# Kernel tuning notes

Measured on AMD Instinct MI355X. Metric: run time of the kernel, lower is better.

The kernel has to match this reference:

```python
import jax, jax.numpy as jnp
import numpy as np

BN_EPS = 1e-5
GRID_W = 17  # conv output width hardcoded via lat_idx*17+lon_idx

def _conv(x, w, b, stride):
    y = jax.lax.conv_general_dilated(x, w, (stride, stride), [(1, 1), (1, 1)],
                                     dimension_numbers=("NCHW", "OIHW", "NCHW"))
    return y + b[None, :, None, None]

def _bn_eval(x, g, b):
    # running_mean=0, running_var=1 (fresh BatchNorm in eval mode)
    inv = jnp.float32(1.0 / np.sqrt(1.0 + BN_EPS))
    return x * (g[None, :, None, None] * inv) + b[None, :, None, None]

def setup_inputs() -> dict:
    key = jax.random.key(0)
    ks = iter(jax.random.split(key, 64))
    def rn(shape, s=0.05):
        return jax.random.normal(next(ks), shape, jnp.float32) * s
    B, S, K = 512, 128, 64
    NR = 100000
    inp = {}
    inp["roads"] = jax.random.randint(next(ks), (B, S), 0, NR)
    inp["ratios"] = jax.random.uniform(next(ks), (B, S), jnp.float32) * 0.9 + 0.1
    inp["T"] = jax.random.normal(next(ks), (1, 1, 138, 138), jnp.float32)
    inp["lon_idx"] = jax.random.randint(next(ks), (B, K), 0, 17)
    inp["lat_idx"] = jax.random.randint(next(ks), (B, K), 0, 17)
    inp["lengths"] = jax.random.uniform(next(ks), (NR,), jnp.float32) * 100.0 + 1.0
    inp["map_u"] = jnp.arange(NR, dtype=jnp.int32)
    inp["map_s1"] = jax.random.randint(next(ks), (NR,), 0, 14)
    inp["map_s2"] = jax.random.randint(next(ks), (NR,), 0, 7)
    inp["map_s3"] = jax.random.randint(next(ks), (NR,), 0, 2)
    inp["emb_u"] = rn((NR, 128))
    inp["emb_s1"] = rn((14, 16)); inp["emb_s2"] = rn((7, 8)); inp["emb_s3"] = rn((2, 4))
    inp["rho_w1"] = rn((156, 512)); inp["rho_b1"] = jnp.zeros((512,), jnp.float32)
    inp["rho_w21"] = rn((512, 128)); inp["rho_b21"] = jnp.zeros((128,), jnp.float32)
    inp["conv1_w"] = rn((32, 1, 5, 5)); inp["conv1_b"] = jnp.zeros((32,), jnp.float32)
    inp["bn1_g"] = jnp.ones((32,), jnp.float32); inp["bn1_b"] = jnp.zeros((32,), jnp.float32)
    inp["conv2_w"] = rn((64, 32, 4, 4)); inp["conv2_b"] = jnp.zeros((64,), jnp.float32)
    inp["bn2_g"] = jnp.ones((64,), jnp.float32); inp["bn2_b"] = jnp.zeros((64,), jnp.float32)
    inp["conv3_w"] = rn((128, 64, 4, 4)); inp["conv3_b"] = jnp.zeros((128,), jnp.float32)
    inp["bn3_g"] = jnp.ones((128,), jnp.float32); inp["bn3_b"] = jnp.zeros((128,), jnp.float32)
    inp["f2_w1"] = rn((128, 256)); inp["f2_b1"] = jnp.zeros((256,), jnp.float32)
    inp["f2_w2"] = rn((256, 128)); inp["f2_b2"] = jnp.zeros((128,), jnp.float32)
    inp["f_w1"] = rn((256, 512)); inp["f_b1"] = jnp.zeros((512,), jnp.float32)
    inp["f_w21"] = rn((512, 1)); inp["f_b21"] = jnp.zeros((1,), jnp.float32)
    inp["f_w22"] = rn((512, 1)); inp["f_b22"] = jnp.zeros((1,), jnp.float32)
    return inp

def reference(roads, ratios, T, lon_idx, lat_idx, lengths, map_u, map_s1, map_s2, map_s3,
              emb_u, emb_s1, emb_s2, emb_s3, rho_w1, rho_b1, rho_w21, rho_b21,
              conv1_w, conv1_b, bn1_g, bn1_b, conv2_w, conv2_b, bn2_g, bn2_b,
              conv3_w, conv3_b, bn3_g, bn3_b, f2_w1, f2_b1, f2_w2, f2_b2,
              f_w1, f_b1, f_w21, f_b21, f_w22, f_b22):
    # road lengths / weights
    road_lens = lengths[roads] * ratios               # (B,S)
    l = road_lens.sum(axis=1)                         # (B,)
    w = road_lens / l[:, None]                        # (B,S)
    # ProbRho (eval: dropout=id, reparameterize -> mu)
    u = emb_u[map_u[roads]]                           # (B,S,128)
    s1 = emb_s1[map_s1[roads]]; s2 = emb_s2[map_s2[roads]]; s3 = emb_s3[map_s3[roads]]
    x = jnp.concatenate([u, s1, s2, s3], axis=2)      # (B,S,156)
    h = jax.nn.relu(x @ rho_w1 + rho_b1)
    rho = h @ rho_w21 + rho_b21                       # (B,S,128)
    # ProbTraffic_spatial conv stack
    t = jax.nn.leaky_relu(_bn_eval(_conv(T, conv1_w, conv1_b, 2), bn1_g, bn1_b), 0.1)
    t = jax.nn.leaky_relu(_bn_eval(_conv(t, conv2_w, conv2_b, 2), bn2_g, bn2_b), 0.1)
    t = jax.nn.leaky_relu(_bn_eval(_conv(t, conv3_w, conv3_b, 2), bn3_g, bn3_b), 0.1)  # (1,128,17,17)
    c_flat = jnp.transpose(t[0], (1, 2, 0)).reshape(-1, t.shape[1])  # (289,128)
    # fused segment gather + mean over each trajectory's grid cells
    idx = lat_idx * GRID_W + lon_idx                  # (B,K)
    c_mean = c_flat[idx].mean(axis=1)                 # (B,128)
    h2 = jax.nn.selu(c_mean @ f2_w1 + f2_b1)
    c2 = h2 @ f2_w2 + f2_b2                           # (B,128)
    # ProbTravelTime
    xcat = jnp.concatenate([rho, jnp.broadcast_to(c2[:, None, :], rho.shape)], axis=2)  # (B,S,256)
    h3 = jax.nn.relu(xcat @ f_w1 + f_b1)              # (B,S,512)
    logm = (h3 @ f_w21 + f_b21)[..., 0]               # (B,S)
    logv = (h3 @ f_w22 + f_b22)[..., 0]
    logw = jnp.log(w)
    logm_agg = jax.nn.logsumexp(logm + logw, axis=1)
    logv_agg = jax.nn.logsumexp(logv + 2.0 * logw, axis=1)
    logl = jnp.log(l)
    logmu = logl - logm_agg
    loglam = logl - 3.0 * logm_agg - logv_agg
    return (logmu, loglam)
```

## Files before the change

kernel.cpp:

```cpp
#include <hip/hip_runtime.h>
#include <hip/hip_bf16.h>
#include <math.h>

#define BB 512
#define SS 128
#define NROWS (BB*SS)
#define TMG 128
#define NBLKG (NROWS/TMG)

__device__ __forceinline__ float leaky01(float x){ return x >= 0.f ? x : 0.1f*x; }

#define BN_INV 0.9999950000374997f
#define SELU_A 1.6732632423543772f
#define SELU_S 1.0507009873554805f

typedef __attribute__((ext_vector_type(8))) short short8;
typedef __attribute__((ext_vector_type(4))) float f32x4;

__device__ __forceinline__ unsigned short f2bf(float f) {
    unsigned int u = __float_as_uint(f);
    u += 0x7fff + ((u >> 16) & 1);
    return (unsigned short)(u >> 16);
}
__device__ __forceinline__ unsigned int pk2(float a, float b) {
    __hip_bfloat162 h = __float22bfloat162_rn(make_float2(a, b));
    unsigned int u;
    __builtin_memcpy(&u, &h, 4);
    return u;
}
__device__ __forceinline__ uint2 pack4bf(float a, float b, float c, float d) {
    uint2 r; r.x = pk2(a, b); r.y = pk2(c, d); return r;
}

__device__ __forceinline__ unsigned short* xsp(unsigned short* base, int row, int col) {
    unsigned off = (unsigned)(row*384 + col*2);
    off ^= (unsigned)((row & 7) << 4);
    return (unsigned short*)((char*)base + off);
}
__device__ __forceinline__ unsigned short* h1p(unsigned short* base, int row, int col) {
    unsigned off = (unsigned)(row*1024 + col*2);
    off ^= (unsigned)((row & 7) << 4);
    return (unsigned short*)((char*)base + off);
}
__device__ __forceinline__ unsigned short* xcp(unsigned short* base, int row, int col) {
    unsigned off = (unsigned)(row*256 + col*2);
    off ^= (unsigned)((row & 7) << 4);
    return (unsigned short*)((char*)base + off);
}

#define PREP_N (278528 + 32768 + 131072)
#define PREP_BLOCKS (PREP_N/256)
#define CONV1_BLOCKS 578

__global__ __launch_bounds__(256) void combo1_kernel(
    const float* __restrict__ w1, const float* __restrict__ w21, const float* __restrict__ fw1,
    unsigned short* __restrict__ sw1, unsigned short* __restrict__ sw21, unsigned short* __restrict__ sw3,
    const float* __restrict__ c2w_in, const float* __restrict__ c3w_in,
    float* __restrict__ w2t, float* __restrict__ w3t,
    const float* __restrict__ T, const float* __restrict__ cw,
    const float* __restrict__ cbias, const float* __restrict__ g,
    const float* __restrict__ bb, float* __restrict__ out)
{
    if (blockIdx.x < PREP_BLOCKS) {
        int t = blockIdx.x*256 + threadIdx.x;
        if (t < 81920) {
            int j = t & 7; int r = t >> 3; int lane = r & 63; r >>= 6;
            int ks = r % 5; int nt = r / 5;
            int n = nt*16 + (lane & 15);
            int k = ks*32 + (lane >> 4)*8 + j;
            float v = (k < 156) ? w1[k*512 + n] : 0.f;
            sw1[t] = f2bf(v);
        } else if (t < 147456) {
            int u = t - 81920;
            int j = u & 7; int r = u >> 3; int lane = r & 63; r >>= 6;
            int ks = r & 15; int nt = r >> 4;
            int d = nt*16 + (lane & 15);
            int k = ks*32 + (lane >> 4)*8 + j;
            sw21[u] = f2bf(w21[k*128 + d]);
        } else if (t < 278528) {
            int u = t - 147456;
            int j = u & 7; int r = u >> 3; int lane = r & 63; r >>= 6;
            int ks = r & 7; int nt = r >> 3;
            int n = nt*16 + (lane & 15);
            int k = ks*32 + (lane >> 4)*8 + j;
            sw3[u] = f2bf(fw1[k*512 + n]);
        } else if (t < 278528 + 32768) {
            int u = t - 278528;
            int oc = u >> 9; int r = u & 511;
            int kk = r >> 5; int ic = r & 31;
            w2t[u] = c2w_in[oc*512 + ic*16 + kk];
        } else {
            int u = t - (278528 + 32768);
            int oc = u >> 10; int r = u & 1023;
            int kk = r >> 6; int ic = r & 63;
            w3t[u] = c3w_in[oc*1024 + ic*16 + kk];
        }
    } else {
        int t = (blockIdx.x - PREP_BLOCKS)*256 + threadIdx.x;
        if (t >= 32*68*68) return;
        int oc  = t & 31;
        int pos = t >> 5;
        int oy = pos / 68, ox = pos % 68;
        float acc = cbias[oc];
        #pragma unroll
        for (int ky=0; ky<5; ++ky) {
            int iy = oy*2 - 1 + ky;
            if (iy < 0 || iy >= 138) continue;
            #pragma unroll
            for (int kx=0; kx<5; ++kx) {
                int ix = ox*2 - 1 + kx;
                if (ix < 0 || ix >= 138) continue;
                acc += cw[oc*25 + ky*5 + kx] * T[iy*138 + ix];
            }
        }
        acc = acc * (g[oc]*BN_INV) + bb[oc];
        out[pos*32 + oc] = leaky01(acc);
    }
}

__global__ __launch_bounds__(256) void conv2_kernel(
    const float* __restrict__ in,
    const float* __restrict__ w2t,
    const float* __restrict__ bias, const float* __restrict__ g,
    const float* __restrict__ bb, float* __restrict__ out)
{
    int gid = blockIdx.x*256 + threadIdx.x;
    if (gid >= 64*34*34*4) return;
    int icg = gid & 3;
    int o   = gid >> 2;
    int oc  = o & 63;
    int pos = o >> 6;
    int oy = pos / 34, ox = pos % 34;
    float acc = 0.f;
    #pragma unroll
    for (int ky=0; ky<4; ++ky) {
        int iy = oy*2 - 1 + ky;
        if (iy < 0 || iy >= 68) continue;
        #pragma unroll
        for (int kx=0; kx<4; ++kx) {
            int ix = ox*2 - 1 + kx;
            if (ix < 0 || ix >= 68) continue;
            const float* ip = &in[(iy*68+ix)*32 + icg*8];
            const float* wp = &w2t[oc*512 + (ky*4+kx)*32 + icg*8];
            float4 i0 = *(const float4*)ip, i1 = *(const float4*)(ip+4);
            float4 w0 = *(const float4*)wp, w1v = *(const float4*)(wp+4);
            acc += i0.x*w0.x + i0.y*w0.y + i0.z*w0.z + i0.w*w0.w
                 + i1.x*w1v.x + i1.y*w1v.y + i1.z*w1v.z + i1.w*w1v.w;
        }
    }
    acc += __shfl_xor(acc, 1, 64);
    acc += __shfl_xor(acc, 2, 64);
    if (icg == 0) {
        acc = (acc + bias[oc]) * (g[oc]*BN_INV) + bb[oc];
        out[pos*64 + oc] = leaky01(acc);
    }
}

__global__ __launch_bounds__(256) void conv3_kernel(
    const float* __restrict__ in,
    const float* __restrict__ w3t,
    const float* __restrict__ bias, const float* __restrict__ g,
    const float* __restrict__ bb, float* __restrict__ outT)
{
    int gid = blockIdx.x*256 + threadIdx.x;
    if (gid >= 128*289*8) return;
    int icg = gid & 7;
    int o   = gid >> 3;
    int oc  = o & 127;
    int pos = o >> 7;
    int oy = pos / 17, ox = pos % 17;
    float acc = 0.f;
    #pragma unroll
    for (int ky=0; ky<4; ++ky) {
        int iy = oy*2 - 1 + ky;
        if (iy < 0 || iy >= 34) continue;
        #pragma unroll
        for (int kx=0; kx<4; ++kx) {
            int ix = ox*2 - 1 + kx;
            if (ix < 0 || ix >= 34) continue;
            const float* ip = &in[(iy*34+ix)*64 + icg*8];
            const float* wp = &w3t[oc*1024 + (ky*4+kx)*64 + icg*8];
            float4 i0 = *(const float4*)ip, i1 = *(const float4*)(ip+4);
            float4 w0 = *(const float4*)wp, w1v = *(const float4*)(wp+4);
            acc += i0.x*w0.x + i0.y*w0.y + i0.z*w0.z + i0.w*w0.w
                 + i1.x*w1v.x + i1.y*w1v.y + i1.z*w1v.z + i1.w*w1v.w;
        }
    }
    acc += __shfl_xor(acc, 1, 64);
    acc += __shfl_xor(acc, 2, 64);
    acc += __shfl_xor(acc, 4, 64);
    if (icg == 0) {
        acc = (acc + bias[oc]) * (g[oc]*BN_INV) + bb[oc];
        outT[pos*128 + oc] = leaky01(acc);
    }
}

__global__ __launch_bounds__(256) void cmh2c2_kernel(
    const float* __restrict__ t3T, const int* __restrict__ lat, const int* __restrict__ lon,
    const float* __restrict__ w1, const float* __restrict__ b1,
    const float* __restrict__ w2, const float* __restrict__ b2,
    const float* __restrict__ fw1, const float* __restrict__ fb1,
    float* __restrict__ cvb)
{
    __shared__ int   ps[64];
    __shared__ float part[256];
    __shared__ float cms[128];
    __shared__ float h2s[256];
    __shared__ float c2s[128];
    const int b = blockIdx.x;
    const int tid = threadIdx.x;
    if (tid < 64) ps[tid] = lat[b*64+tid]*17 + lon[b*64+tid];
    __syncthreads();
    {
        int d = tid & 127, half = tid >> 7;
        float s = 0.f;
        #pragma unroll 8
        for (int k=0; k<32; ++k) s += t3T[ps[half*32+k]*128 + d];
        part[tid] = s;
    }
    __syncthreads();
    if (tid < 128) cms[tid] = (part[tid] + part[tid+128]) * (1.f/64.f);
    __syncthreads();
    {
        float acc = b1[tid];
        #pragma unroll 8
        for (int k=0; k<128; ++k) acc += cms[k] * w1[k*256 + tid];
        h2s[tid] = acc > 0.f ? SELU_S*acc : SELU_S*SELU_A*(expf(acc)-1.f);
    }
    __syncthreads();
    {
        int d = tid & 127, half = tid >> 7;
        float acc = 0.f;
        #pragma unroll 8
        for (int k=0; k<128; ++k) acc += h2s[half*128 + k] * w2[(half*128+k)*128 + d];
        part[tid] = acc;
    }
    __syncthreads();
    if (tid < 128) c2s[tid] = part[tid] + part[tid+128] + b2[tid];
    __syncthreads();
    {
        float a0 = fb1[tid], a1 = fb1[tid + 256];
        #pragma unroll 8
        for (int k=0; k<128; ++k) {
            float c = c2s[k];
            a0 += c * fw1[(128+k)*512 + tid];
            a1 += c * fw1[(128+k)*512 + 256 + tid];
        }
        cvb[b*512 + tid]       = a0;
        cvb[b*512 + 256 + tid] = a1;
    }
}

__global__ __launch_bounds__(1024, 4) void mega_kernel(
    const int* __restrict__ roads, const float* __restrict__ ratios,
    const float* __restrict__ lengths,
    const int* __restrict__ map_u, const int* __restrict__ map_s1,
    const int* __restrict__ map_s2, const int* __restrict__ map_s3,
    const float* __restrict__ emb_u, const float* __restrict__ emb_s1,
    const float* __restrict__ emb_s2, const float* __restrict__ emb_s3,
    const unsigned short* __restrict__ sw1, const float* __restrict__ b1,
    const unsigned short* __restrict__ sw21, const float* __restrict__ b21,
    const unsigned short* __restrict__ sw3, const float* __restrict__ cvb,
    const float* __restrict__ fw21, const float* __restrict__ fb21,
    const float* __restrict__ fw22, const float* __restrict__ fb22,
    float* __restrict__ out)
{
    __shared__ unsigned short buf[65536];
    float* pmv = (float*)buf;
    float* fin = (float*)buf + 4096;

    const int tid  = threadIdx.x;
    const int wid  = tid >> 6;
    const int lane = tid & 63;
    const int lo   = lane & 15;
    const int hi   = lane >> 4;
    const int b    = blockIdx.x;
    const int r0   = b * TMG;
    const int nt2  = wid >> 1;
    const int rh   = wid & 1;

    short8 afp00 = *(const short8*)&sw1[((wid*2+0)*5 + 0)*512 + lane*8];
    short8 afp10 = *(const short8*)&sw1[((wid*2+1)*5 + 0)*512 + lane*8];
    short8 afp01 = *(const short8*)&sw1[((wid*2+0)*5 + 1)*512 + lane*8];
    short8 afp11 = *(const short8*)&sw1[((wid*2+1)*5 + 1)*512 + lane*8];

    {
        int row = tid >> 3, seg = tid & 7;
        int road = roads[r0 + row];
        const float* src = emb_u + (long)map_u[road]*128 + seg*16;
        #pragma unroll
        for (int i=0;i<4;++i) {
            float4 v = *(const float4*)&src[i*4];
            *(uint2*)xsp(buf, row, seg*16 + i*4) = pack4bf(v.x, v.y, v.z, v.w);
        }
    }
    for (int idx = tid; idx < 128*32; idx += 1024) {
        int row = idx >> 5, k2 = idx & 31;
        int road = roads[r0 + row];
        float v;
        if      (k2 < 16) v = emb_s1[map_s1[road]*16 + k2];
        else if (k2 < 24) v = emb_s2[map_s2[road]*8  + (k2-16)];
        else if (k2 < 28) v = emb_s3[map_s3[road]*4  + (k2-24)];
        else              v = 0.f;
        *xsp(buf, row, 128 + k2) = f2bf(v);
    }
    __syncthreads();

    f32x4 acc1[2][8];
    {
        #pragma unroll
        for (int mt=0;mt<2;++mt)
            #pragma unroll
            for (int rg=0;rg<8;++rg) acc1[mt][rg]=(f32x4)(0.f);
        short8 a0c = afp00, a1c = afp10, a0n = afp01, a1n = afp11;
        #pragma unroll
        for (int ks=0; ks<5; ++ks) {
            short8 a0f = a0c, a1f = a1c;
            if (ks < 3) {
                a0f = *(const short8*)&sw1[((wid*2+0)*5 + ks+2)*512 + lane*8];
                a1f = *(const short8*)&sw1[((wid*2+1)*5 + ks+2)*512 + lane*8];
            }
            const int kb = ks*32 + hi*8;
            short8 bf[4];
            #pragma unroll
            for (int rg=0;rg<4;++rg) bf[rg] = *(const short8*)xsp(buf, rg*16+lo, kb);
            #pragma unroll
            for (int rg=0;rg<4;++rg) {
                acc1[0][rg] = __builtin_amdgcn_mfma_f32_16x16x32_bf16(a0c, bf[rg], acc1[0][rg], 0,0,0);
                acc1[1][rg] = __builtin_amdgcn_mfma_f32_16x16x32_bf16(a1c, bf[rg], acc1[1][rg], 0,0,0);
            }
            #pragma unroll
            for (int rg=0;rg<4;++rg) bf[rg] = *(const short8*)xsp(buf, (4+rg)*16+lo, kb);
            #pragma unroll
            for (int rg=0;rg<4;++rg) {
                acc1[0][4+rg] = __builtin_amdgcn_mfma_f32_16x16x32_bf16(a0c, bf[rg], acc1[0][4+rg], 0,0,0);
                acc1[1][4+rg] = __builtin_amdgcn_mfma_f32_16x16x32_bf16(a1c, bf[rg], acc1[1][4+rg], 0,0,0);
            }
            a0c = a0n; a1c = a1n; a0n = a0f; a1n = a1f;
        }
    }
    __syncthreads();

    short8 a2q0, a2q1, a2q2, a2q3;
    {
        a2q0 = *(const short8*)&sw21[(nt2*16 + 0)*512 + lane*8];
        a2q1 = *(const short8*)&sw21[(nt2*16 + 1)*512 + lane*8];
        a2q2 = *(const short8*)&sw21[(nt2*16 + 2)*512 + lane*8];
        a2q3 = *(const short8*)&sw21[(nt2*16 + 3)*512 + lane*8];
        const int n0 = wid * 32;
        #pragma unroll
        for (int mt=0;mt<2;++mt) {
            const int nb = n0 + mt*16 + hi*4;
            float4 bias = *(const float4*)&b1[nb];
            const float* bp = (const float*)&bias;
            #pragma unroll
            for (int rg=0;rg<8;++rg) {
                const float* a = (const float*)&acc1[mt][rg];
                float y0 = fmaxf(a[0]+bp[0], 0.f), y1 = fmaxf(a[1]+bp[1], 0.f);
                float y2 = fmaxf(a[2]+bp[2], 0.f), y3 = fmaxf(a[3]+bp[3], 0.f);
                *(uint2*)h1p(buf, rg*16+lo, nb) = pack4bf(y0,y1,y2,y3);
            }
        }
    }
    __syncthreads();

    f32x4 acc2[4];
    {
        #pragma unroll
        for (int i=0;i<4;++i) acc2[i]=(f32x4)(0.f);
        #pragma unroll
        for (int ks=0; ks<16; ++ks) {
            short8 a_use = a2q0;
            a2q0 = a2q1; a2q1 = a2q2; a2q2 = a2q3;
            if (ks < 12)
                a2q3 = *(const short8*)&sw21[(nt2*16 + ks+4)*512 + lane*8];
            const int kb = ks*32 + hi*8;
            short8 bf[4];
            #pragma unroll
            for (int i=0;i<4;++i) bf[i] = *(const short8*)h1p(buf, (rh*4+i)*16+lo, kb);
            #pragma unroll
            for (int i=0;i<4;++i)
                acc2[i] = __builtin_amdgcn_mfma_f32_16x16x32_bf16(a_use, bf[i], acc2[i], 0,0,0);
        }
    }
    __syncthreads();

    short8 a3c0, a3c1, a3n0, a3n1;
    {
        a3c0 = *(const short8*)&sw3[((wid*2+0)*8 + 0)*512 + lane*8];
        a3c1 = *(const short8*)&sw3[((wid*2+1)*8 + 0)*512 + lane*8];
        a3n0 = *(const short8*)&sw3[((wid*2+0)*8 + 1)*512 + lane*8];
        a3n1 = *(const short8*)&sw3[((wid*2+1)*8 + 1)*512 + lane*8];
        const int nb = nt2*16 + hi*4;
        float4 bias = *(const float4*)&b21[nb];
        const float* bp = (const float*)&bias;
        #pragma unroll
        for (int i=0;i<4;++i) {
            const float* a = (const float*)&acc2[i];
            *(uint2*)xcp(buf, (rh*4+i)*16+lo, nb) =
                pack4bf(a[0]+bp[0], a[1]+bp[1], a[2]+bp[2], a[3]+bp[3]);
        }
    }
    __syncthreads();

    float sm[8], sv[8];
    {
        const int n0 = wid * 32;
        f32x4 acc[2][8];
        #pragma unroll
        for (int mt=0;mt<2;++mt)
            #pragma unroll
            for (int rg=0;rg<8;++rg) acc[mt][rg]=(f32x4)(0.f);
        #pragma unroll
        for (int ks=0; ks<4; ++ks) {
            short8 c0f = a3c0, c1f = a3c1;
            if (ks < 2) {
                c0f = *(const short8*)&sw3[((wid*2+0)*8 + ks+2)*512 + lane*8];
                c1f = *(const short8*)&sw3[((wid*2+1)*8 + ks+2)*512 + lane*8];
            }
            const int kb = ks*32 + hi*8;
            short8 bf[4];
            #pragma unroll
            for (int rg=0;rg<4;++rg) bf[rg] = *(const short8*)xcp(buf, rg*16+lo, kb);
            #pragma unroll
            for (int rg=0;rg<4;++rg) {
                acc[0][rg] = __builtin_amdgcn_mfma_f32_16x16x32_bf16(a3c0, bf[rg], acc[0][rg], 0,0,0);
                acc[1][rg] = __builtin_amdgcn_mfma_f32_16x16x32_bf16(a3c1, bf[rg], acc[1][rg], 0,0,0);
            }
            #pragma unroll
            for (int rg=0;rg<4;++rg) bf[rg] = *(const short8*)xcp(buf, (4+rg)*16+lo, kb);
            #pragma unroll
            for (int rg=0;rg<4;++rg) {
                acc[0][4+rg] = __builtin_amdgcn_mfma_f32_16x16x32_bf16(a3c0, bf[rg], acc[0][4+rg], 0,0,0);
                acc[1][4+rg] = __builtin_amdgcn_mfma_f32_16x16x32_bf16(a3c1, bf[rg], acc[1][4+rg], 0,0,0);
            }
            a3c0 = a3n0; a3c1 = a3n1; a3n0 = c0f; a3n1 = c1f;
        }
        #pragma unroll
        for (int rg=0;rg<8;++rg){ sm[rg]=0.f; sv[rg]=0.f; }
        #pragma unroll
        for (int mt=0;mt<2;++mt) {
            const int nb = n0 + mt*16 + hi*4;
            float4 bias = *(const float4*)&cvb[b*512 + nb];
            float4 wm   = *(const float4*)&fw21[nb];
            float4 wv   = *(const float4*)&fw22[nb];
            const float *bp=(const float*)&bias, *wmp=(const float*)&wm, *wvp=(const float*)&wv;
            #pragma unroll
            for (int rg=0;rg<8;++rg) {
                const float* a = (const float*)&acc[mt][rg];
                #pragma unroll
                for (int j=0;j<4;++j) {
                    float y = fmaxf(a[j]+bp[j], 0.f);
                    sm[rg] += y*wmp[j];
                    sv[rg] += y*wvp[j];
                }
            }
        }
        #pragma unroll
        for (int rg=0;rg<8;++rg) {
            sm[rg] += __shfl_xor(sm[rg], 16, 64); sm[rg] += __shfl_xor(sm[rg], 32, 64);
            sv[rg] += __shfl_xor(sv[rg], 16, 64); sv[rg] += __shfl_xor(sv[rg], 32, 64);
        }
    }
    __syncthreads();
    if (hi == 0) {
        #pragma unroll
        for (int rg=0;rg<8;++rg) {
            pmv[wid*128 + rg*16 + lo]        = sm[rg];
            pmv[2048 + wid*128 + rg*16 + lo] = sv[rg];
        }
    }
    __syncthreads();

    float rl = 0.f, am = 0.f, av = 0.f;
    if (tid < 128) {
        float s_m = 0.f, s_v = 0.f;
        #pragma unroll
        for (int w=0; w<16; ++w) {
            s_m += pmv[w*128 + tid];
            s_v += pmv[2048 + w*128 + tid];
        }
        s_m += fb21[0]; s_v += fb22[0];
        int gi = r0 + tid;
        rl = lengths[roads[gi]] * ratios[gi];
        float ws = rl;
        #pragma unroll
        for (int off=32; off; off>>=1) ws += __shfl_xor(ws, off, 64);
        if (lane == 0) fin[wid] = ws;
        am = s_m; av = s_v;
    }
    __syncthreads();
    if (tid < 128) {
        float l = fin[0] + fin[1];
        float logl = logf(l);
        float lw = logf(rl) - logl;
        am += lw; av += 2.f*lw;
        float mm = am, mv = av;
        #pragma unroll
        for (int off=32; off; off>>=1) { mm = fmaxf(mm, __shfl_xor(mm, off, 64)); mv = fmaxf(mv, __shfl_xor(mv, off, 64)); }
        if (lane == 0) { fin[2+wid] = mm; fin[4+wid] = mv; fin[8+wid] = logl; }
    }
    __syncthreads();
    if (tid < 128) {
        float mm = fmaxf(fin[2], fin[3]);
        float mv = fmaxf(fin[4], fin[5]);
        float se = expf(am - mm), sev = expf(av - mv);
        #pragma unroll
        for (int off=32; off; off>>=1) { se += __shfl_xor(se, off, 64); sev += __shfl_xor(sev, off, 64); }
        if (lane == 0) { fin[10+wid] = se; fin[12+wid] = sev; }
    }
    __syncthreads();
    if (tid == 0) {
        float mm = fmaxf(fin[2], fin[3]);
        float mv = fmaxf(fin[4], fin[5]);
        float lsem = logf(fin[10] + fin[11]) + mm;
        float lsev = logf(fin[12] + fin[13]) + mv;
        float logl = fin[8];
        out[b]       = logl - lsem;
        out[512 + b] = logl - 3.f*lsem - lsev;
    }
}

extern "C" void kernel_launch(void* const* d_in, const int* in_sizes, int n_in,
                              void* d_out, int out_size, void* d_ws, size_t ws_size,
                              hipStream_t stream) {
    const int*   roads   = (const int*)  d_in[0];
    const float* ratios  = (const float*)d_in[1];
    const float* T       = (const float*)d_in[2];
    const int*   lon_idx = (const int*)  d_in[3];
    const int*   lat_idx = (const int*)  d_in[4];
    const float* lengths = (const float*)d_in[5];
    const int*   map_u   = (const int*)  d_in[6];
    const int*   map_s1  = (const int*)  d_in[7];
    const int*   map_s2  = (const int*)  d_in[8];
    const int*   map_s3  = (const int*)  d_in[9];
    const float* emb_u   = (const float*)d_in[10];
    const float* emb_s1  = (const float*)d_in[11];
    const float* emb_s2  = (const float*)d_in[12];
    const float* emb_s3  = (const float*)d_in[13];
    const float* rho_w1  = (const float*)d_in[14];
    const float* rho_b1  = (const float*)d_in[15];
    const float* rho_w21 = (const float*)d_in[16];
    const float* rho_b21 = (const float*)d_in[17];
    const float* conv1_w = (const float*)d_in[18];
    const float* conv1_b = (const float*)d_in[19];
    const float* bn1_g   = (const float*)d_in[20];
    const float* bn1_b   = (const float*)d_in[21];
    const float* conv2_w = (const float*)d_in[22];
    const float* conv2_b = (const float*)d_in[23];
    const float* bn2_g   = (const float*)d_in[24];
    const float* bn2_b   = (const float*)d_in[25];
    const float* conv3_w = (const float*)d_in[26];
    const float* conv3_b = (const float*)d_in[27];
    const float* bn3_g   = (const float*)d_in[28];
    const float* bn3_b   = (const float*)d_in[29];
    const float* f2_w1   = (const float*)d_in[30];
    const float* f2_b1   = (const float*)d_in[31];
    const float* f2_w2   = (const float*)d_in[32];
    const float* f2_b2   = (const float*)d_in[33];
    const float* f_w1    = (const float*)d_in[34];
    const float* f_b1    = (const float*)d_in[35];
    const float* f_w21   = (const float*)d_in[36];
    const float* f_b21   = (const float*)d_in[37];
    const float* f_w22   = (const float*)d_in[38];
    const float* f_b22   = (const float*)d_in[39];

    float* ws    = (float*)d_ws;
    float* t1    = ws;
    float* t2    = t1 + 147968;
    float* t3T   = t2 + 73984;
    float* cvb   = t3T + 36992;
    float* w2t   = cvb + 262144;
    float* w3t   = w2t + 32768;
    unsigned short* sw1  = (unsigned short*)(w3t + 131072);
    unsigned short* sw21 = sw1 + 81920;
    unsigned short* sw3  = sw21 + 65536;

    combo1_kernel<<<PREP_BLOCKS + CONV1_BLOCKS, 256, 0, stream>>>(
        rho_w1, rho_w21, f_w1, sw1, sw21, sw3,
        conv2_w, conv3_w, w2t, w3t,
        T, conv1_w, conv1_b, bn1_g, bn1_b, t1);
    conv2_kernel<<<(64*34*34*4 + 255)/256, 256, 0, stream>>>(t1, w2t, conv2_b, bn2_g, bn2_b, t2);
    conv3_kernel<<<(128*289*8 + 255)/256, 256, 0, stream>>>(t2, w3t, conv3_b, bn3_g, bn3_b, t3T);
    cmh2c2_kernel<<<512, 256, 0, stream>>>(t3T, lat_idx, lon_idx, f2_w1, f2_b1, f2_w2, f2_b2,
                                           f_w1, f_b1, cvb);
    mega_kernel<<<NBLKG, 1024, 0, stream>>>(roads, ratios, lengths,
                                            map_u, map_s1, map_s2, map_s3,
                                            emb_u, emb_s1, emb_s2, emb_s3,
                                            sw1, rho_b1, sw21, rho_b21,
                                            sw3, cvb, f_w21, f_b21, f_w22, f_b22,
                                            (float*)d_out);
}
```

Measured before the change: 117.1 us.

## Retile per-wave MFMA work into square 64x64 output tiles across GEMMs

Each wave now computes a 4x4 tile of 16x16 outputs (four weight fragments by four row groups, covering half the 128 rows) instead of 2 weight fragments across all 8 row groups. GEMM2 switches to a 2x2 tile per wave. This cuts LDS B-fragment reads per MFMA, since each loaded fragment is reused by four weight fragments. The cross-wave partial reduction and scratch layout are reindexed to match. The trade-off is more weight-fragment registers in flight and a reworked prefetch schedule.

```diff
diff --git a/kernel.cpp b/kernel.cpp
--- a/kernel.cpp
+++ b/kernel.cpp
@@ -267,7 +267,7 @@
 {
     __shared__ unsigned short buf[65536];
     float* pmv = (float*)buf;
-    float* fin = (float*)buf + 4096;
+    float* fin = (float*)buf + 2048;
 
     const int tid  = threadIdx.x;
     const int wid  = tid >> 6;
@@ -276,13 +276,15 @@
     const int hi   = lane >> 4;
     const int b    = blockIdx.x;
     const int r0   = b * TMG;
-    const int nt2  = wid >> 1;
-    const int rh   = wid & 1;
-
-    short8 afp00 = *(const short8*)&sw1[((wid*2+0)*5 + 0)*512 + lane*8];
-    short8 afp10 = *(const short8*)&sw1[((wid*2+1)*5 + 0)*512 + lane*8];
-    short8 afp01 = *(const short8*)&sw1[((wid*2+0)*5 + 1)*512 + lane*8];
-    short8 afp11 = *(const short8*)&sw1[((wid*2+1)*5 + 1)*512 + lane*8];
+    const int ntg  = wid >> 1;
+    const int rhalf= wid & 1;
+    const int ntg2 = wid & 3;
+    const int rq   = wid >> 2;
+
+    short8 afc[4];
+    #pragma unroll
+    for (int mt=0;mt<4;++mt)
+        afc[mt] = *(const short8*)&sw1[((ntg*4+mt)*5 + 0)*512 + lane*8];
 
     {
         int row = tid >> 3, seg = tid & 7;
@@ -306,179 +308,177 @@
     }
     __syncthreads();
 
-    f32x4 acc1[2][8];
-    {
-        #pragma unroll
-        for (int mt=0;mt<2;++mt)
-            #pragma unroll
-            for (int rg=0;rg<8;++rg) acc1[mt][rg]=(f32x4)(0.f);
-        short8 a0c = afp00, a1c = afp10, a0n = afp01, a1n = afp11;
+    f32x4 acc1[4][4];
+    {
+        #pragma unroll
+        for (int mt=0;mt<4;++mt)
+            #pragma unroll
+            for (int rt=0;rt<4;++rt) acc1[mt][rt]=(f32x4)(0.f);
         #pragma unroll
         for (int ks=0; ks<5; ++ks) {
-            short8 a0f = a0c, a1f = a1c;
-            if (ks < 3) {
-                a0f = *(const short8*)&sw1[((wid*2+0)*5 + ks+2)*512 + lane*8];
-                a1f = *(const short8*)&sw1[((wid*2+1)*5 + ks+2)*512 + lane*8];
+            short8 afn[4];
+            if (ks < 4) {
+                #pragma unroll
+                for (int mt=0;mt<4;++mt)
+                    afn[mt] = *(const short8*)&sw1[((ntg*4+mt)*5 + ks+1)*512 + lane*8];
             }
             const int kb = ks*32 + hi*8;
             short8 bf[4];
             #pragma unroll
-            for (int rg=0;rg<4;++rg) bf[rg] = *(const short8*)xsp(buf, rg*16+lo, kb);
-            #pragma unroll
-            for (int rg=0;rg<4;++rg) {
-                acc1[0][rg] = __builtin_amdgcn_mfma_f32_16x16x32_bf16(a0c, bf[rg], acc1[0][rg], 0,0,0);
-                acc1[1][rg] = __builtin_amdgcn_mfma_f32_16x16x32_bf16(a1c, bf[rg], acc1[1][rg], 0,0,0);
-            }
-            #pragma unroll
-            for (int rg=0;rg<4;++rg) bf[rg] = *(const short8*)xsp(buf, (4+rg)*16+lo, kb);
-            #pragma unroll
-            for (int rg=0;rg<4;++rg) {
-                acc1[0][4+rg] = __builtin_amdgcn_mfma_f32_16x16x32_bf16(a0c, bf[rg], acc1[0][4+rg], 0,0,0);
-                acc1[1][4+rg] = __builtin_amdgcn_mfma_f32_16x16x32_bf16(a1c, bf[rg], acc1[1][4+rg], 0,0,0);
-            }
-            a0c = a0n; a1c = a1n; a0n = a0f; a1n = a1f;
-        }
-    }
-    __syncthreads();
-
-    short8 a2q0, a2q1, a2q2, a2q3;
-    {
-        a2q0 = *(const short8*)&sw21[(nt2*16 + 0)*512 + lane*8];
-        a2q1 = *(const short8*)&sw21[(nt2*16 + 1)*512 + lane*8];
-        a2q2 = *(const short8*)&sw21[(nt2*16 + 2)*512 + lane*8];
-        a2q3 = *(const short8*)&sw21[(nt2*16 + 3)*512 + lane*8];
-        const int n0 = wid * 32;
-        #pragma unroll
-        for (int mt=0;mt<2;++mt) {
-            const int nb = n0 + mt*16 + hi*4;
+            for (int rt=0;rt<4;++rt)
+                bf[rt] = *(const short8*)xsp(buf, (rhalf*4+rt)*16+lo, kb);
+            #pragma unroll
+            for (int mt=0;mt<4;++mt)
+                #pragma unroll
+                for (int rt=0;rt<4;++rt)
+                    acc1[mt][rt] = __builtin_amdgcn_mfma_f32_16x16x32_bf16(afc[mt], bf[rt], acc1[mt][rt], 0,0,0);
+            if (ks < 4) {
+                #pragma unroll
+                for (int mt=0;mt<4;++mt) afc[mt] = afn[mt];
+            }
+        }
+    }
+    __syncthreads();
+
+    short8 a2c0, a2c1, a2n0, a2n1;
+    {
+        a2c0 = *(const short8*)&sw21[((ntg2*2+0)*16 + 0)*512 + lane*8];
+        a2c1 = *(const short8*)&sw21[((ntg2*2+1)*16 + 0)*512 + lane*8];
+        a2n0 = *(const short8*)&sw21[((ntg2*2+0)*16 + 1)*512 + lane*8];
+        a2n1 = *(const short8*)&sw21[((ntg2*2+1)*16 + 1)*512 + lane*8];
+        #pragma unroll
+        for (int mt=0;mt<4;++mt) {
+            const int nb = (ntg*4+mt)*16 + hi*4;
             float4 bias = *(const float4*)&b1[nb];
             const float* bp = (const float*)&bias;
             #pragma unroll
-            for (int rg=0;rg<8;++rg) {
-                const float* a = (const float*)&acc1[mt][rg];
+            for (int rt=0;rt<4;++rt) {
+                const float* a = (const float*)&acc1[mt][rt];
                 float y0 = fmaxf(a[0]+bp[0], 0.f), y1 = fmaxf(a[1]+bp[1], 0.f);
                 float y2 = fmaxf(a[2]+bp[2], 0.f), y3 = fmaxf(a[3]+bp[3], 0.f);
-                *(uint2*)h1p(buf, rg*16+lo, nb) = pack4bf(y0,y1,y2,y3);
-            }
-        }
-    }
-    __syncthreads();
-
-    f32x4 acc2[4];
-    {
-        #pragma unroll
-        for (int i=0;i<4;++i) acc2[i]=(f32x4)(0.f);
-        #pragma unroll
+                *(uint2*)h1p(buf, (rhalf*4+rt)*16+lo, nb) = pack4bf(y0,y1,y2,y3);
+            }
+        }
+    }
+    __syncthreads();
+
+    f32x4 acc2[2][2];
+    {
+        acc2[0][0]=(f32x4)(0.f); acc2[0][1]=(f32x4)(0.f);
+        acc2[1][0]=(f32x4)(0.f); acc2[1][1]=(f32x4)(0.f);
+        #pragma unroll 4
         for (int ks=0; ks<16; ++ks) {
-            short8 a_use = a2q0;
-            a2q0 = a2q1; a2q1 = a2q2; a2q2 = a2q3;
-            if (ks < 12)
-                a2q3 = *(const short8*)&sw21[(nt2*16 + ks+4)*512 + lane*8];
+            short8 u0 = a2c0, u1 = a2c1;
+            a2c0 = a2n0; a2c1 = a2n1;
+            if (ks < 14) {
+                a2n0 = *(const short8*)&sw21[((ntg2*2+0)*16 + ks+2)*512 + lane*8];
+                a2n1 = *(const short8*)&sw21[((ntg2*2+1)*16 + ks+2)*512 + lane*8];
+            }
+            const int kb = ks*32 + hi*8;
+            short8 bf0 = *(const short8*)h1p(buf, (rq*2+0)*16+lo, kb);
+            short8 bf1 = *(const short8*)h1p(buf, (rq*2+1)*16+lo, kb);
+            acc2[0][0] = __builtin_amdgcn_mfma_f32_16x16x32_bf16(u0, bf0, acc2[0][0], 0,0,0);
+            acc2[0][1] = __builtin_amdgcn_mfma_f32_16x16x32_bf16(u0, bf1, acc2[0][1], 0,0,0);
+            acc2[1][0] = __builtin_amdgcn_mfma_f32_16x16x32_bf16(u1, bf0, acc2[1][0], 0,0,0);
+            acc2[1][1] = __builtin_amdgcn_mfma_f32_16x16x32_bf16(u1, bf1, acc2[1][1], 0,0,0);
+        }
+    }
+    __syncthreads();
+
+    short8 a3c[4];
+    {
+        #pragma unroll
+        for (int mt=0;mt<4;++mt)
+            a3c[mt] = *(const short8*)&sw3[((ntg*4+mt)*8 + 0)*512 + lane*8];
+        #pragma unroll
+        for (int mt=0;mt<2;++mt) {
+            const int nb = (ntg2*2+mt)*16 + hi*4;
+            float4 bias = *(const float4*)&b21[nb];
+            const float* bp = (const float*)&bias;
+            #pragma unroll
+            for (int rt=0;rt<2;++rt) {
+                const float* a = (const float*)&acc2[mt][rt];
+                *(uint2*)xcp(buf, (rq*2+rt)*16+lo, nb) =
+                    pack4bf(a[0]+bp[0], a[1]+bp[1], a[2]+bp[2], a[3]+bp[3]);
+            }
+        }
+    }
+    __syncthreads();
+
+    float sm[4], sv[4];
+    {
+        f32x4 acc[4][4];
+        #pragma unroll
+        for (int mt=0;mt<4;++mt)
+            #pragma unroll
+            for (int rt=0;rt<4;++rt) acc[mt][rt]=(f32x4)(0.f);
+        #pragma unroll
+        for (int ks=0; ks<4; ++ks) {
+            short8 a3n[4];
+            if (ks < 3) {
+                #pragma unroll
+                for (int mt=0;mt<4;++mt)
+                    a3n[mt] = *(const short8*)&sw3[((ntg*4+mt)*8 + ks+1)*512 + lane*8];
+            }
             const int kb = ks*32 + hi*8;
             short8 bf[4];
             #pragma unroll
-            for (int i=0;i<4;++i) bf[i] = *(const short8*)h1p(buf, (rh*4+i)*16+lo, kb);
-            #pragma unroll
-            for (int i=0;i<4;++i)
-                acc2[i] = __builtin_amdgcn_mfma_f32_16x16x32_bf16(a_use, bf[i], acc2[i], 0,0,0);
-        }
-    }
-    __syncthreads();
-
-    short8 a3c0, a3c1, a3n0, a3n1;
-    {
-        a3c0 = *(const short8*)&sw3[((wid*2+0)*8 + 0)*512 + lane*8];
-        a3c1 = *(const short8*)&sw3[((wid*2+1)*8 + 0)*512 + lane*8];
-        a3n0 = *(const short8*)&sw3[((wid*2+0)*8 + 1)*512 + lane*8];
-        a3n1 = *(const short8*)&sw3[((wid*2+1)*8 + 1)*512 + lane*8];
-        const int nb = nt2*16 + hi*4;
-        float4 bias = *(const float4*)&b21[nb];
-        const float* bp = (const float*)&bias;
-        #pragma unroll
-        for (int i=0;i<4;++i) {
-            const float* a = (const float*)&acc2[i];
-            *(uint2*)xcp(buf, (rh*4+i)*16+lo, nb) =
-                pack4bf(a[0]+bp[0], a[1]+bp[1], a[2]+bp[2], a[3]+bp[3]);
-        }
-    }
-    __syncthreads();
-
-    float sm[8], sv[8];
-    {
-        const int n0 = wid * 32;
-        f32x4 acc[2][8];
-        #pragma unroll
-        for (int mt=0;mt<2;++mt)
-            #pragma unroll
-            for (int rg=0;rg<8;++rg) acc[mt][rg]=(f32x4)(0.f);
-        #pragma unroll
-        for (int ks=0; ks<4; ++ks) {
-            short8 c0f = a3c0, c1f = a3c1;
-            if (ks < 2) {
-                c0f = *(const short8*)&sw3[((wid*2+0)*8 + ks+2)*512 + lane*8];
-                c1f = *(const short8*)&sw3[((wid*2+1)*8 + ks+2)*512 + lane*8];
-            }
-            const int kb = ks*32 + hi*8;
-            short8 bf[4];
-            #pragma unroll
-            for (int rg=0;rg<4;++rg) bf[rg] = *(const short8*)xcp(buf, rg*16+lo, kb);
-            #pragma unroll
-            for (int rg=0;rg<4;++rg) {
-                acc[0][rg] = __builtin_amdgcn_mfma_f32_16x16x32_bf16(a3c0, bf[rg], acc[0][rg], 0,0,0);
-                acc[1][rg] = __builtin_amdgcn_mfma_f32_16x16x32_bf16(a3c1, bf[rg], acc[1][rg], 0,0,0);
-            }
-            #pragma unroll
-            for (int rg=0;rg<4;++rg) bf[rg] = *(const short8*)xcp(buf, (4+rg)*16+lo, kb);
-            #pragma unroll
-            for (int rg=0;rg<4;++rg) {
-                acc[0][4+rg] = __builtin_amdgcn_mfma_f32_16x16x32_bf16(a3c0, bf[rg], acc[0][4+rg], 0,0,0);
-                acc[1][4+rg] = __builtin_amdgcn_mfma_f32_16x16x32_bf16(a3c1, bf[rg], acc[1][4+rg], 0,0,0);
-            }
-            a3c0 = a3n0; a3c1 = a3n1; a3n0 = c0f; a3n1 = c1f;
-        }
-        #pragma unroll
-        for (int rg=0;rg<8;++rg){ sm[rg]=0.f; sv[rg]=0.f; }
-        #pragma unroll
-        for (int mt=0;mt<2;++mt) {
-            const int nb = n0 + mt*16 + hi*4;
+            for (int rt=0;rt<4;++rt)
+                bf[rt] = *(const short8*)xcp(buf, (rhalf*4+rt)*16+lo, kb);
+            #pragma unroll
+            for (int mt=0;mt<4;++mt)
+                #pragma unroll
+                for (int rt=0;rt<4;++rt)
+                    acc[mt][rt] = __builtin_amdgcn_mfma_f32_16x16x32_bf16(a3c[mt], bf[rt], acc[mt][rt], 0,0,0);
+            if (ks < 3) {
+                #pragma unroll
+                for (int mt=0;mt<4;++mt) a3c[mt] = a3n[mt];
+            }
+        }
+        #pragma unroll
+        for (int rt=0;rt<4;++rt){ sm[rt]=0.f; sv[rt]=0.f; }
+        #pragma unroll
+        for (int mt=0;mt<4;++mt) {
+            const int nb = (ntg*4+mt)*16 + hi*4;
             float4 bias = *(const float4*)&cvb[b*512 + nb];
             float4 wm   = *(const float4*)&fw21[nb];
             float4 wv   = *(const float4*)&fw22[nb];
             const float *bp=(const float*)&bias, *wmp=(const float*)&wm, *wvp=(const float*)&wv;
             #pragma unroll
-            for (int rg=0;rg<8;++rg) {
-                const float* a = (const float*)&acc[mt][rg];
+            for (int rt=0;rt<4;++rt) {
+                const float* a = (const float*)&acc[mt][rt];
                 #pragma unroll
                 for (int j=0;j<4;++j) {
                     float y = fmaxf(a[j]+bp[j], 0.f);
-                    sm[rg] += y*wmp[j];
-                    sv[rg] += y*wvp[j];
+                    sm[rt] += y*wmp[j];
+                    sv[rt] += y*wvp[j];
                 }
             }
         }
         #pragma unroll
-        for (int rg=0;rg<8;++rg) {
-            sm[rg] += __shfl_xor(sm[rg], 16, 64); sm[rg] += __shfl_xor(sm[rg], 32, 64);
-            sv[rg] += __shfl_xor(sv[rg], 16, 64); sv[rg] += __shfl_xor(sv[rg], 32, 64);
+        for (int rt=0;rt<4;++rt) {
+            sm[rt] += __shfl_xor(sm[rt], 16, 64); sm[rt] += __shfl_xor(sm[rt], 32, 64);
+            sv[rt] += __shfl_xor(sv[rt], 16, 64); sv[rt] += __shfl_xor(sv[rt], 32, 64);
         }
     }
     __syncthreads();
     if (hi == 0) {
         #pragma unroll
-        for (int rg=0;rg<8;++rg) {
-            pmv[wid*128 + rg*16 + lo]        = sm[rg];
-            pmv[2048 + wid*128 + rg*16 + lo] = sv[rg];
+        for (int rt=0;rt<4;++rt) {
+            pmv[wid*64 + rt*16 + lo]        = sm[rt];
+            pmv[1024 + wid*64 + rt*16 + lo] = sv[rt];
         }
     }
     __syncthreads();
 
     float rl = 0.f, am = 0.f, av = 0.f;
     if (tid < 128) {
+        const int rhr = tid >> 6, rr = tid & 63;
         float s_m = 0.f, s_v = 0.f;
         #pragma unroll
-        for (int w=0; w<16; ++w) {
-            s_m += pmv[w*128 + tid];
-            s_v += pmv[2048 + w*128 + tid];
+        for (int k=0; k<8; ++k) {
+            s_m += pmv[(k*2+rhr)*64 + rr];
+            s_v += pmv[1024 + (k*2+rhr)*64 + rr];
         }
         s_m += fb21[0]; s_v += fb22[0];
         int gi = r0 + tid;
```

After: 128.8 us. 1.1x slower.

## Batch four trajectories per block in cmh2c2 to reuse weight loads

Applied to the files above, without the earlier changes.

The grid-feature MLP kernel now handles four batch rows per block, so each weight element loaded from global memory is reused across four accumulators instead of being re-read by 512 separate blocks. This cuts weight traffic for the f2_w1, f2_w2 and f_w1 matvecs by about four times, in exchange for fewer blocks (128) and more registers per thread. Separately, mega_kernel's launch bounds minimum-blocks hint is lowered from 4 to 2, which lets the compiler use more registers per thread at the cost of occupancy.

```diff
diff --git a/kernel.cpp b/kernel.cpp
--- a/kernel.cpp
+++ b/kernel.cpp
@@ -195,6 +195,7 @@
     }
 }
 
+#define BPB 4
 __global__ __launch_bounds__(256) void cmh2c2_kernel(
     const float* __restrict__ t3T, const int* __restrict__ lat, const int* __restrict__ lon,
     const float* __restrict__ w1, const float* __restrict__ b1,
@@ -202,56 +203,87 @@
     const float* __restrict__ fw1, const float* __restrict__ fb1,
     float* __restrict__ cvb)
 {
-    __shared__ int   ps[64];
-    __shared__ float part[256];
-    __shared__ float cms[128];
-    __shared__ float h2s[256];
-    __shared__ float c2s[128];
-    const int b = blockIdx.x;
+    __shared__ int   ps[BPB*64];
+    __shared__ float cms[BPB*128];
+    __shared__ float h2s[BPB*256];
+    __shared__ float part[BPB*2*128];
+    __shared__ float c2s[BPB*128];
+    const int b0 = blockIdx.x * BPB;
     const int tid = threadIdx.x;
-    if (tid < 64) ps[tid] = lat[b*64+tid]*17 + lon[b*64+tid];
-    __syncthreads();
-    {
-        int d = tid & 127, half = tid >> 7;
+    if (tid < BPB*64) {
+        int bl = tid >> 6, k = tid & 63;
+        ps[tid] = lat[(b0+bl)*64+k]*17 + lon[(b0+bl)*64+k];
+    }
+    __syncthreads();
+    #pragma unroll
+    for (int it=0; it<BPB/2; ++it) {
+        int idx = tid + it*256;
+        int bl = idx >> 7, d = idx & 127;
         float s = 0.f;
         #pragma unroll 8
-        for (int k=0; k<32; ++k) s += t3T[ps[half*32+k]*128 + d];
-        part[tid] = s;
-    }
-    __syncthreads();
-    if (tid < 128) cms[tid] = (part[tid] + part[tid+128]) * (1.f/64.f);
-    __syncthreads();
-    {
-        float acc = b1[tid];
-        #pragma unroll 8
-        for (int k=0; k<128; ++k) acc += cms[k] * w1[k*256 + tid];
-        h2s[tid] = acc > 0.f ? SELU_S*acc : SELU_S*SELU_A*(expf(acc)-1.f);
+        for (int k=0; k<64; ++k) s += t3T[ps[bl*64+k]*128 + d];
+        cms[bl*128 + d] = s * (1.f/64.f);
+    }
+    __syncthreads();
+    {
+        int n = tid;
+        float acc[BPB];
+        float bb0 = b1[n];
+        #pragma unroll
+        for (int bl=0;bl<BPB;++bl) acc[bl] = bb0;
+        for (int k=0; k<128; ++k) {
+            float w = w1[k*256 + n];
+            #pragma unroll
+            for (int bl=0;bl<BPB;++bl) acc[bl] += cms[bl*128+k] * w;
+        }
+        #pragma unroll
+        for (int bl=0;bl<BPB;++bl)
+            h2s[bl*256 + n] = acc[bl] > 0.f ? SELU_S*acc[bl] : SELU_S*SELU_A*(expf(acc[bl])-1.f);
     }
     __syncthreads();
     {
         int d = tid & 127, half = tid >> 7;
-        float acc = 0.f;
-        #pragma unroll 8
-        for (int k=0; k<128; ++k) acc += h2s[half*128 + k] * w2[(half*128+k)*128 + d];
-        part[tid] = acc;
-    }
-    __syncthreads();
-    if (tid < 128) c2s[tid] = part[tid] + part[tid+128] + b2[tid];
-    __syncthreads();
-    {
-        float a0 = fb1[tid], a1 = fb1[tid + 256];
-        #pragma unroll 8
+        float acc[BPB];
+        #pragma unroll
+        for (int bl=0;bl<BPB;++bl) acc[bl] = 0.f;
         for (int k=0; k<128; ++k) {
-            float c = c2s[k];
-            a0 += c * fw1[(128+k)*512 + tid];
-            a1 += c * fw1[(128+k)*512 + 256 + tid];
-        }
-        cvb[b*512 + tid]       = a0;
-        cvb[b*512 + 256 + tid] = a1;
-    }
-}
-
-__global__ __launch_bounds__(1024, 4) void mega_kernel(
+            float w = w2[(half*128+k)*128 + d];
+            #pragma unroll
+            for (int bl=0;bl<BPB;++bl) acc[bl] += h2s[bl*256 + half*128 + k] * w;
+        }
+        #pragma unroll
+        for (int bl=0;bl<BPB;++bl) part[(bl*2+half)*128 + d] = acc[bl];
+    }
+    __syncthreads();
+    for (int idx = tid; idx < BPB*128; idx += 256) {
+        int bl = idx >> 7, d = idx & 127;
+        c2s[idx] = part[(bl*2+0)*128 + d] + part[(bl*2+1)*128 + d] + b2[d];
+    }
+    __syncthreads();
+    {
+        float a0[BPB], a1[BPB];
+        float f0 = fb1[tid], f1 = fb1[tid + 256];
+        #pragma unroll
+        for (int bl=0;bl<BPB;++bl){ a0[bl]=f0; a1[bl]=f1; }
+        for (int k=0; k<128; ++k) {
+            float w0 = fw1[(128+k)*512 + tid];
+            float w1v= fw1[(128+k)*512 + 256 + tid];
+            #pragma unroll
+            for (int bl=0;bl<BPB;++bl) {
+                float c = c2s[bl*128+k];
+                a0[bl] += c * w0;
+                a1[bl] += c * w1v;
+            }
+        }
+        #pragma unroll
+        for (int bl=0;bl<BPB;++bl) {
+            cvb[(b0+bl)*512 + tid]       = a0[bl];
+            cvb[(b0+bl)*512 + 256 + tid] = a1[bl];
+        }
+    }
+}
+
+__global__ __launch_bounds__(1024, 2) void mega_kernel(
     const int* __restrict__ roads, const float* __restrict__ ratios,
     const float* __restrict__ lengths,
     const int* __restrict__ map_u, const int* __restrict__ map_s1,
@@ -582,8 +614,8 @@
         T, conv1_w, conv1_b, bn1_g, bn1_b, t1);
     conv2_kernel<<<(64*34*34*4 + 255)/256, 256, 0, stream>>>(t1, w2t, conv2_b, bn2_g, bn2_b, t2);
     conv3_kernel<<<(128*289*8 + 255)/256, 256, 0, stream>>>(t2, w3t, conv3_b, bn3_g, bn3_b, t3T);
-    cmh2c2_kernel<<<512, 256, 0, stream>>>(t3T, lat_idx, lon_idx, f2_w1, f2_b1, f2_w2, f2_b2,
-                                           f_w1, f_b1, cvb);
+    cmh2c2_kernel<<<512/BPB, 256, 0, stream>>>(t3T, lat_idx, lon_idx, f2_w1, f2_b1, f2_w2, f2_b2,
+                                               f_w1, f_b1, cvb);
     mega_kernel<<<NBLKG, 1024, 0, stream>>>(roads, ratios, lengths,
                                             map_u, map_s1, map_s2, map_s3,
                                             emb_u, emb_s1, emb_s2, emb_s3,
```

Measured after the change: 120.7 us. 3.1% more time.
